# Optimization experiments

Hardware: AMD Instinct MI355X
Metric: run time of the kernel (lower is better)

The kernel has to match this reference:

```python
import jax, jax.numpy as jnp
import numpy as np

NUM_USERS = 100000
NUM_ITEMS = 200000
EMB_DIM = 64
NUM_LAYERS = 3
NUM_INTER = 1000000
BATCH = 16384


def setup_inputs() -> dict:
    key = jax.random.key(0)
    k1, k2, k3, k4, k5, k6, k7 = jax.random.split(key, 7)
    # xavier-uniform-ish init for embeddings
    bound_u = float(np.sqrt(6.0 / (NUM_USERS + EMB_DIM)))
    bound_i = float(np.sqrt(6.0 / (NUM_ITEMS + EMB_DIM)))
    user_emb = jax.random.uniform(k1, (NUM_USERS, EMB_DIM), jnp.float32, -bound_u, bound_u)
    item_emb = jax.random.uniform(k2, (NUM_ITEMS, EMB_DIM), jnp.float32, -bound_i, bound_i)
    layer_weights = jax.random.uniform(k3, (NUM_LAYERS + 1,), jnp.float32)
    inter_users = jax.random.randint(k4, (NUM_INTER,), 0, NUM_USERS, jnp.int32)
    inter_items = jax.random.randint(k5, (NUM_INTER,), 0, NUM_ITEMS, jnp.int32)
    user_ids = jax.random.randint(k6, (BATCH,), 0, NUM_USERS, jnp.int32)
    item_ids = jax.random.randint(k7, (BATCH,), 0, NUM_ITEMS, jnp.int32)
    return {
        "user_emb": user_emb,
        "item_emb": item_emb,
        "layer_weights": layer_weights,
        "inter_users": inter_users,
        "inter_items": inter_items,
        "user_ids": user_ids,
        "item_ids": item_ids,
    }


def reference(user_emb, item_emb, layer_weights, inter_users, inter_items, user_ids, item_ids):
    n_users = user_emb.shape[0]
    n_items = item_emb.shape[0]
    n_nodes = n_users + n_items

    # Symmetrized bipartite edge list: (u -> i+n_users) and (i+n_users -> u)
    rows = inter_users
    cols = inter_items + n_users
    src = jnp.concatenate([rows, cols])  # [2E]
    dst = jnp.concatenate([cols, rows])  # [2E]

    # Symmetric degree normalization: D^{-1/2} A D^{-1/2}
    deg = jax.ops.segment_sum(jnp.ones_like(src, dtype=jnp.float32), src,
                              num_segments=n_nodes)
    dinv = jnp.where(deg > 0, jax.lax.rsqrt(jnp.maximum(deg, 1.0)) * (deg > 0), 0.0)
    dinv = jnp.where(deg > 0, deg ** -0.5, 0.0)
    edge_w = dinv[src] * dinv[dst]  # [2E]

    emb = jnp.concatenate([user_emb, item_emb], axis=0)  # [N, D]
    weights = jax.nn.softmax(layer_weights)

    final = weights[0] * emb
    for layer in range(NUM_LAYERS):
        # SpMM: out[src] += w * emb[dst]
        emb = jax.ops.segment_sum(edge_w[:, None] * emb[dst], src,
                                  num_segments=n_nodes)
        final = final + weights[layer + 1] * emb

    u_final = final[:n_users]
    i_final = final[n_users:]

    user_vectors = u_final[user_ids]   # [B, D]
    item_vectors = i_final[item_ids]   # [B, D]
    scores = jnp.sum(user_vectors * item_vectors, axis=1)  # [B]
    return scores
```

## Files before the change

kernel.cpp:

```cpp
#include <hip/hip_runtime.h>
#include <math.h>

#define NUM_USERS 100000
#define NUM_ITEMS 200000
#define N_NODES   300000
#define EMB       64
#define NUM_INTER 1000000
#define MAX_SLOTS (2 * NUM_INTER + 3 * N_NODES + 16)
#define BATCH     16384

#define BSHIFT 9
#define BNODES 512
#define NBKT   ((N_NODES + BNODES - 1) / BNODES)
#define CAP    6144
#define EDGES_PER_BLOCK 4096
#define AB_BLOCKS ((NUM_INTER + EDGES_PER_BLOCK - 1) / EDGES_PER_BLOCK)
#define QMARK_BLOCKS ((BATCH * 2) / 256)

#define CONV_BLOCKS ((N_NODES * 8 + 255) / 256)
#define PROP_BLOCKS ((N_NODES * 8 + 255) / 256)

typedef int      vint4 __attribute__((ext_vector_type(4)));
typedef _Float16 half8 __attribute__((ext_vector_type(8)));

#define PMASK 0x7FFFFu

__global__ __launch_bounds__(256) void bucket_scatter_k(
        const int* __restrict__ iu, const int* __restrict__ ii,
        const int* __restrict__ uid, const int* __restrict__ iid,
        int* __restrict__ cursor , unsigned* __restrict__ pairs,
        unsigned char* __restrict__ qflag, int* __restrict__ flag) {
    int tid = threadIdx.x;
    if (blockIdx.x < QMARK_BLOCKS) {
        int t = blockIdx.x * 256 + tid;
        int node = (t & 1) ? (NUM_USERS + iid[t >> 1]) : uid[t >> 1];
        qflag[node] = 1;
        flag[node]  = 1;
        return;
    }
    __shared__ int hist[NBKT];
    __shared__ int gbase[NBKT];
    int bid = blockIdx.x - QMARK_BLOCKS;
    for (int b = tid; b < NBKT; b += 256) hist[b] = 0;
    __syncthreads();

    int e0 = bid * EDGES_PER_BLOCK;
    int u[16], it[16];
    unsigned pk[32];
    #pragma unroll
    for (int k = 0; k < 16; ++k) {
        int e = e0 + k * 256 + tid;
        bool v = (e < NUM_INTER);
        u[k]  = v ? iu[e] : -1;
        it[k] = v ? (NUM_USERS + ii[e]) : -1;
    }
    #pragma unroll
    for (int k = 0; k < 16; ++k) {
        if (u[k] >= 0) {
            int b0 = u[k] >> BSHIFT;
            int r0 = atomicAdd(&hist[b0], 1);
            pk[2 * k] = ((unsigned)b0 << 13) | (unsigned)r0;
            int b1 = it[k] >> BSHIFT;
            int r1 = atomicAdd(&hist[b1], 1);
            pk[2 * k + 1] = ((unsigned)b1 << 13) | (unsigned)r1;
        }
    }
    __syncthreads();
    for (int b = tid; b < NBKT; b += 256) {
        int c = hist[b];
        if (c) gbase[b] = atomicAdd(&cursor[b * 16], c);
    }
    __syncthreads();
    #pragma unroll
    for (int k = 0; k < 16; ++k) {
        if (u[k] >= 0) {
            unsigned p0 = pk[2 * k];
            int b0 = (int)(p0 >> 13);
            int s0 = gbase[b0] + (int)(p0 & 0x1fffu);
            if (s0 < CAP)
                pairs[(size_t)b0 * CAP + s0] =
                    ((unsigned)(u[k] & (BNODES - 1)) << 19) | (unsigned)it[k];
            unsigned p1 = pk[2 * k + 1];
            int b1 = (int)(p1 >> 13);
            int s1 = gbase[b1] + (int)(p1 & 0x1fffu);
            if (s1 < CAP)
                pairs[(size_t)b1 * CAP + s1] =
                    ((unsigned)(it[k] & (BNODES - 1)) << 19) | (unsigned)u[k];
        }
    }
}

__global__ __launch_bounds__(256) void bucket_deg_k(
        const int* __restrict__ cursor, const unsigned* __restrict__ pairs,
        const unsigned char* __restrict__ qflag, int* __restrict__ flag,
        int* __restrict__ deg, float* __restrict__ dinv, float* __restrict__ d2,
        float* __restrict__ rcp, int* __restrict__ lofs, int* __restrict__ bkt_padded) {
    __shared__ int cnt[BNODES];
    __shared__ int sc[256];
    __shared__ unsigned qf[BNODES / 4];
    int b = blockIdx.x, tid = threadIdx.x;
    cnt[tid] = 0; cnt[tid + 256] = 0;
    if (tid < BNODES / 4)
        qf[tid] = ((const unsigned*)(qflag + ((size_t)b << BSHIFT)))[tid];
    __syncthreads();
    int n = cursor[b * 16]; if (n > CAP) n = CAP;
    const unsigned* p = pairs + (size_t)b * CAP;
    const unsigned char* qfb = (const unsigned char*)qf;
    for (int j = tid; j < n; j += 256) {
        unsigned code = p[j];
        int l = (int)(code >> 19);
        atomicAdd(&cnt[l], 1);
        if (qfb[l]) flag[code & PMASK] = 1;
    }
    __syncthreads();

    int l0 = 2 * tid, l1 = 2 * tid + 1;
    int c0 = cnt[l0], c1 = cnt[l1];
    int p0 = (c0 + 3) & ~3, p1 = (c1 + 3) & ~3;
    int s = p0 + p1;
    sc[tid] = s;
    __syncthreads();
    for (int o = 1; o < 256; o <<= 1) {
        int x = (tid >= o) ? sc[tid - o] : 0;
        __syncthreads();
        sc[tid] += x;
        __syncthreads();
    }
    int excl = sc[tid] - s;
    int g0 = (b << BSHIFT) + l0;
    int g1 = g0 + 1;
    if (g0 < N_NODES) {
        deg[g0] = c0;
        float fd = (float)c0;
        dinv[g0] = (c0 > 0) ? (1.0f / sqrtf(fd)) : 0.0f;
        d2[g0]   = (c0 > 0) ? (1.0f / fd) : 0.0f;
        rcp[g0]  = (c0 > 0) ? sqrtf(fd) : 0.0f;
        lofs[g0] = excl;
    }
    if (g1 < N_NODES) {
        deg[g1] = c1;
        float fd = (float)c1;
        dinv[g1] = (c1 > 0) ? (1.0f / sqrtf(fd)) : 0.0f;
        d2[g1]   = (c1 > 0) ? (1.0f / fd) : 0.0f;
        rcp[g1]  = (c1 > 0) ? sqrtf(fd) : 0.0f;
        lofs[g1] = excl + p0;
    }
    if (tid == 255) bkt_padded[b] = sc[255];
}

__global__ void csr_mid_k(const int* __restrict__ bkt_padded, int* __restrict__ bkt_base,
                          int* __restrict__ row_start,
                          const float* __restrict__ lw, float* __restrict__ w,
                          _Float16* __restrict__ semb, _Float16* __restrict__ z1,
                          _Float16* __restrict__ z2) {
    __shared__ int lds[1024];
    int t = threadIdx.x;
    int v = (t < NBKT) ? bkt_padded[t] : 0;
    lds[t] = v;
    __syncthreads();
    for (int o = 1; o < 1024; o <<= 1) {
        int x = (t >= o) ? lds[t - o] : 0;
        __syncthreads();
        lds[t] += x;
        __syncthreads();
    }
    if (t < NBKT) bkt_base[t] = lds[t] - v;
    if (t == 1023) row_start[N_NODES] = lds[1023];
    if (t < 96) {
        unsigned* p = (t < 32) ? (unsigned*)semb : (t < 64) ? (unsigned*)z1 : (unsigned*)z2;
        p[(size_t)N_NODES * 32 + (t & 31)] = 0u;
    }
    if (t == 0) {
        float a = lw[0], b = lw[1], c = lw[2], d = lw[3];
        float m = fmaxf(fmaxf(a, b), fmaxf(c, d));
        float e0 = expf(a - m), e1 = expf(b - m), e2 = expf(c - m), e3 = expf(d - m);
        float sm = e0 + e1 + e2 + e3;
        w[0] = e0 / sm; w[1] = e1 / sm; w[2] = e2 / sm; w[3] = e3 / sm;
    }
}

__global__ __launch_bounds__(256) void bucket_build_k(
        const int* __restrict__ cursor, const unsigned* __restrict__ pairs,
        const int* __restrict__ bkt_base, const int* __restrict__ lofs,
        int* __restrict__ row_start, int* __restrict__ nbr,
        const float* __restrict__ dinv,
        const float* __restrict__ ue, const float* __restrict__ ie,
        _Float16* __restrict__ semb) {
    int bid = blockIdx.x;
    int tid = threadIdx.x;
    if (bid >= NBKT) {
        int t = (bid - NBKT) * 256 + tid;
        int node = t >> 3;
        int q = t & 7;
        if (node >= N_NODES) return;
        const float4* src = (node < NUM_USERS)
            ? (const float4*)ue + (size_t)node * 16
            : (const float4*)ie + (size_t)(node - NUM_USERS) * 16;
        float4 f0 = src[q * 2];
        float4 f1 = src[q * 2 + 1];
        float s = dinv[node];
        half8 h;
        h[0] = (_Float16)(s * f0.x); h[1] = (_Float16)(s * f0.y);
        h[2] = (_Float16)(s * f0.z); h[3] = (_Float16)(s * f0.w);
        h[4] = (_Float16)(s * f1.x); h[5] = (_Float16)(s * f1.y);
        h[6] = (_Float16)(s * f1.z); h[7] = (_Float16)(s * f1.w);
        ((half8*)semb)[(size_t)node * 8 + q] = h;
        return;
    }
    __shared__ int ofs[BNODES];
    __shared__ int cnt2[BNODES];
    int b = bid;
    int base = bkt_base[b];
    {
        int g0 = (b << BSHIFT) + tid;
        int g1 = g0 + 256;
        int o0 = (g0 < N_NODES) ? lofs[g0] : 0;
        int o1 = (g1 < N_NODES) ? lofs[g1] : 0;
        ofs[tid] = o0; ofs[tid + 256] = o1;
        cnt2[tid] = 0; cnt2[tid + 256] = 0;
        if (g0 < N_NODES) row_start[g0] = base + o0;
        if (g1 < N_NODES) row_start[g1] = base + o1;
    }
    __syncthreads();
    int n = cursor[b * 16]; if (n > CAP) n = CAP;
    const unsigned* p = pairs + (size_t)b * CAP;
    for (int j = tid; j < n; j += 256) {
        unsigned code = p[j];
        int l = (int)(code >> 19);
        int r = atomicAdd(&cnt2[l], 1);
        nbr[base + ofs[l] + r] = (int)(code & PMASK);
    }
}

__global__ void prop_first_k(const int* __restrict__ row_start, const int* __restrict__ nbr,
                             const int* __restrict__ deg, const float* __restrict__ d2,
                             const _Float16* __restrict__ semb, _Float16* __restrict__ z1) {
    int t = blockIdx.x * blockDim.x + threadIdx.x;
    int node = t >> 3;
    int q = t & 7;
    if (node >= N_NODES) return;
    int beg = row_start[node], end = row_start[node + 1];
    int lim = beg + deg[node];
    const half8* src = (const half8*)semb;
    float a0 = 0.f, a1 = 0.f, a2 = 0.f, a3 = 0.f, a4 = 0.f, a5 = 0.f, a6 = 0.f, a7 = 0.f;
    for (int j = beg; j < end; j += 8) {
        vint4 na = __builtin_nontemporal_load((const vint4*)(nbr + j));
        vint4 nb = __builtin_nontemporal_load((const vint4*)(nbr + j + 4));
        #pragma unroll
        for (int k = 0; k < 8; ++k) {
            int id = (j + k < lim) ? ((k < 4) ? na[k] : nb[k - 4]) : N_NODES;
            half8 h = src[(size_t)id * 8 + q];
            a0 += (float)h[0]; a1 += (float)h[1]; a2 += (float)h[2]; a3 += (float)h[3];
            a4 += (float)h[4]; a5 += (float)h[5]; a6 += (float)h[6]; a7 += (float)h[7];
        }
    }
    float s = d2[node];
    half8 r;
    r[0] = (_Float16)(s * a0); r[1] = (_Float16)(s * a1);
    r[2] = (_Float16)(s * a2); r[3] = (_Float16)(s * a3);
    r[4] = (_Float16)(s * a4); r[5] = (_Float16)(s * a5);
    r[6] = (_Float16)(s * a6); r[7] = (_Float16)(s * a7);
    __builtin_nontemporal_store(r, (half8*)z1 + (size_t)node * 8 + q);
}

__global__ void prop_masked_k(const int* __restrict__ row_start, const int* __restrict__ nbr,
                              const int* __restrict__ deg, const float* __restrict__ d2,
                              const int* __restrict__ flag,
                              const _Float16* __restrict__ in, _Float16* __restrict__ out) {
    int t = blockIdx.x * blockDim.x + threadIdx.x;
    int node = t >> 3;
    int q = t & 7;
    if (node >= N_NODES) return;
    if (!flag[node]) return;
    int beg = row_start[node], end = row_start[node + 1];
    int lim = beg + deg[node];
    const half8* src = (const half8*)in;
    float a0 = 0.f, a1 = 0.f, a2 = 0.f, a3 = 0.f, a4 = 0.f, a5 = 0.f, a6 = 0.f, a7 = 0.f;
    for (int j = beg; j < end; j += 8) {
        vint4 na = __builtin_nontemporal_load((const vint4*)(nbr + j));
        vint4 nb = __builtin_nontemporal_load((const vint4*)(nbr + j + 4));
        #pragma unroll
        for (int k = 0; k < 8; ++k) {
            int id = (j + k < lim) ? ((k < 4) ? na[k] : nb[k - 4]) : N_NODES;
            half8 h = src[(size_t)id * 8 + q];
            a0 += (float)h[0]; a1 += (float)h[1]; a2 += (float)h[2]; a3 += (float)h[3];
            a4 += (float)h[4]; a5 += (float)h[5]; a6 += (float)h[6]; a7 += (float)h[7];
        }
    }
    float s = d2[node];
    half8 r;
    r[0] = (_Float16)(s * a0); r[1] = (_Float16)(s * a1);
    r[2] = (_Float16)(s * a2); r[3] = (_Float16)(s * a3);
    r[4] = (_Float16)(s * a4); r[5] = (_Float16)(s * a5);
    r[6] = (_Float16)(s * a6); r[7] = (_Float16)(s * a7);
    __builtin_nontemporal_store(r, (half8*)out + (size_t)node * 8 + q);
}

__global__ void fused_score_k(const int* __restrict__ row_start, const int* __restrict__ nbr,
                              const int* __restrict__ deg,
                              const float* __restrict__ dinv, const float* __restrict__ rcp,
                              const float* __restrict__ ue, const float* __restrict__ ie,
                              const _Float16* __restrict__ z1, const _Float16* __restrict__ z2,
                              const int* __restrict__ uid, const int* __restrict__ iid,
                              const float* __restrict__ w4, float* __restrict__ out) {
    int t = blockIdx.x * blockDim.x + threadIdx.x;
    int slot = t >> 4;
    if (slot >= BATCH) return;
    int within = t & 15;
    int side = within >> 3;
    int q = within & 7;

    int node;
    const float4* erow;
    if (side == 0) {
        int u = uid[slot];
        node = u;
        erow = (const float4*)ue + (size_t)u * 16;
    } else {
        int ii_ = iid[slot];
        node = NUM_USERS + ii_;
        erow = (const float4*)ie + (size_t)ii_ * 16;
    }

    float w0 = w4[0], w1 = w4[1], w2 = w4[2], w3 = w4[3];
    int beg = row_start[node], end = row_start[node + 1];
    int lim = beg + deg[node];
    const half8* z2v = (const half8*)z2;

    float a0 = 0.f, a1 = 0.f, a2 = 0.f, a3 = 0.f, a4 = 0.f, a5 = 0.f, a6 = 0.f, a7 = 0.f;
    for (int j = beg; j < end; j += 8) {
        vint4 na = __builtin_nontemporal_load((const vint4*)(nbr + j));
        vint4 nb = __builtin_nontemporal_load((const vint4*)(nbr + j + 4));
        #pragma unroll
        for (int k = 0; k < 8; ++k) {
            int id = (j + k < lim) ? ((k < 4) ? na[k] : nb[k - 4]) : N_NODES;
            half8 h = z2v[(size_t)id * 8 + q];
            a0 += (float)h[0]; a1 += (float)h[1]; a2 += (float)h[2]; a3 += (float)h[3];
            a4 += (float)h[4]; a5 += (float)h[5]; a6 += (float)h[6]; a7 += (float)h[7];
        }
    }

    float r  = rcp[node];
    float di = dinv[node];
    float e[8];
    *reinterpret_cast<float4*>(&e[0]) = erow[q * 2];
    *reinterpret_cast<float4*>(&e[4]) = erow[q * 2 + 1];
    half8 h1 = ((const half8*)z1)[(size_t)node * 8 + q];
    half8 h2 = z2v[(size_t)node * 8 + q];
    float acc[8] = {a0, a1, a2, a3, a4, a5, a6, a7};

    float f[8];
    #pragma unroll
    for (int d = 0; d < 8; ++d)
        f[d] = w0 * e[d] + r * (w1 * (float)h1[d] + w2 * (float)h2[d]) + w3 * di * acc[d];

    float p = 0.f;
    #pragma unroll
    for (int d = 0; d < 8; ++d) {
        float o = __shfl_xor(f[d], 8);
        p += f[d] * o;
    }
    p += __shfl_xor(p, 1);
    p += __shfl_xor(p, 2);
    p += __shfl_xor(p, 4);

    if (within == 0) out[slot] = p;
}


extern "C" void kernel_launch(void* const* d_in, const int* in_sizes, int n_in,
                              void* d_out, int out_size, void* d_ws, size_t ws_size,
                              hipStream_t stream) {
    const float* user_emb = (const float*)d_in[0];
    const float* item_emb = (const float*)d_in[1];
    const float* layer_w  = (const float*)d_in[2];
    const int*   inter_u  = (const int*)d_in[3];
    const int*   inter_i  = (const int*)d_in[4];
    const int*   user_ids = (const int*)d_in[5];
    const int*   item_ids = (const int*)d_in[6];
    float* out = (float*)d_out;

    char* base = (char*)d_ws;
    size_t off = 0;
    auto alloc = [&](size_t bytes) -> char* {
        char* p = base + off;
        off = (off + bytes + 255) & ~(size_t)255;
        return p;
    };
    float*    w4        = (float*)    alloc(4 * sizeof(float));
    int*      deg       = (int*)      alloc((size_t)N_NODES * sizeof(int));
    float*    dinv      = (float*)    alloc((size_t)N_NODES * sizeof(float));
    float*    d2        = (float*)    alloc((size_t)N_NODES * sizeof(float));
    float*    rcp       = (float*)    alloc((size_t)N_NODES * sizeof(float));
    int*      lofs      = (int*)      alloc((size_t)N_NODES * sizeof(int));
    int*      row_start = (int*)      alloc(((size_t)N_NODES + 1) * sizeof(int));
    int*      bkt_pad   = (int*)      alloc((size_t)NBKT * sizeof(int));
    int*      bkt_base  = (int*)      alloc((size_t)NBKT * sizeof(int));
    int*           flag   = (int*)          alloc((size_t)N_NODES * sizeof(int));
    unsigned char* qflag  = (unsigned char*)alloc((size_t)N_NODES + 512);
    int*           cursor = (int*)          alloc((size_t)NBKT * 16 * sizeof(int));
    unsigned* pairs     = (unsigned*) alloc((size_t)NBKT * CAP * sizeof(unsigned));
    int*      csr_nbr   = (int*)      alloc((size_t)MAX_SLOTS * sizeof(int));
    _Float16* semb      = (_Float16*) alloc(((size_t)N_NODES + 1) * EMB * sizeof(_Float16));
    _Float16* zA        = (_Float16*) alloc(((size_t)N_NODES + 1) * EMB * sizeof(_Float16));
    _Float16* zB        = (_Float16*) alloc(((size_t)N_NODES + 1) * EMB * sizeof(_Float16));

    size_t span = (size_t)((char*)cursor - (char*)flag) + (size_t)NBKT * 16 * sizeof(int);
    hipMemsetAsync(flag, 0, span, stream);

    bucket_scatter_k<<<QMARK_BLOCKS + AB_BLOCKS, 256, 0, stream>>>(
        inter_u, inter_i, user_ids, item_ids, cursor, pairs, qflag, flag);

    bucket_deg_k<<<NBKT, 256, 0, stream>>>(
        cursor, pairs, qflag, flag, deg, dinv, d2, rcp, lofs, bkt_pad);

    csr_mid_k<<<1, 1024, 0, stream>>>(bkt_pad, bkt_base, row_start, layer_w, w4, semb, zB, zA);

    bucket_build_k<<<NBKT + CONV_BLOCKS, 256, 0, stream>>>(
        cursor, pairs, bkt_base, lofs, row_start, csr_nbr, dinv, user_emb, item_emb, semb);

    prop_first_k<<<PROP_BLOCKS, 256, 0, stream>>>(
        row_start, csr_nbr, deg, d2, semb, zB);

    prop_masked_k<<<PROP_BLOCKS, 256, 0, stream>>>(
        row_start, csr_nbr, deg, d2, flag, zB, zA);

    fused_score_k<<<(BATCH * 16 + 255) / 256, 256, 0, stream>>>(
        row_start, csr_nbr, deg, dinv, rcp, user_emb, item_emb,
        zB , zA , user_ids, item_ids, w4, out);
}
```

Before: 271.9 us.

## Fuse CSR build stages into one per-bucket kernel with fixed bucket slot regions

Merges the degree, global scan, CSR build and embedding-conversion kernels into a single per-bucket kernel. Each bucket now gets a fixed 8192-slot region in the neighbour array, so the global prefix scan over buckets is no longer needed. The softmax and padding-row init move into an extra block of the scatter kernel, and the flag array shrinks from int to byte. This removes two launches and the intermediate lofs, bkt_pad and bkt_base arrays, at the cost of a sparser neighbour array and a per-bucket neighbour overflow risk past 8192 padded slots. It also drops the nontemporal stores and derives row end from the degree.

After: 267.5 us. No clear change (-1.6%).

```diff
diff --git a/kernel.cpp b/kernel.cpp
--- a/kernel.cpp
+++ b/kernel.cpp
@@ -6,18 +6,18 @@
 #define N_NODES   300000
 #define EMB       64
 #define NUM_INTER 1000000
-#define MAX_SLOTS (2 * NUM_INTER + 3 * N_NODES + 16)
 #define BATCH     16384
 
 #define BSHIFT 9
 #define BNODES 512
 #define NBKT   ((N_NODES + BNODES - 1) / BNODES)
 #define CAP    6144
+#define RSHIFT 13
+#define RSLOTS (1 << RSHIFT)
 #define EDGES_PER_BLOCK 4096
 #define AB_BLOCKS ((NUM_INTER + EDGES_PER_BLOCK - 1) / EDGES_PER_BLOCK)
 #define QMARK_BLOCKS ((BATCH * 2) / 256)
 
-#define CONV_BLOCKS ((N_NODES * 8 + 255) / 256)
 #define PROP_BLOCKS ((N_NODES * 8 + 255) / 256)
 
 typedef int      vint4 __attribute__((ext_vector_type(4)));
@@ -29,7 +29,9 @@
         const int* __restrict__ iu, const int* __restrict__ ii,
         const int* __restrict__ uid, const int* __restrict__ iid,
         int* __restrict__ cursor , unsigned* __restrict__ pairs,
-        unsigned char* __restrict__ qflag, int* __restrict__ flag) {
+        unsigned char* __restrict__ qflag, unsigned char* __restrict__ flag,
+        const float* __restrict__ lw, float* __restrict__ w4,
+        _Float16* __restrict__ semb, _Float16* __restrict__ z1, _Float16* __restrict__ z2) {
     int tid = threadIdx.x;
     if (blockIdx.x < QMARK_BLOCKS) {
         int t = blockIdx.x * 256 + tid;
@@ -38,9 +40,23 @@
         flag[node]  = 1;
         return;
     }
+    if (blockIdx.x == QMARK_BLOCKS) {
+        if (tid < 96) {
+            unsigned* p = (tid < 32) ? (unsigned*)semb : (tid < 64) ? (unsigned*)z1 : (unsigned*)z2;
+            p[(size_t)N_NODES * 32 + (tid & 31)] = 0u;
+        }
+        if (tid == 0) {
+            float a = lw[0], b = lw[1], c = lw[2], d = lw[3];
+            float m = fmaxf(fmaxf(a, b), fmaxf(c, d));
+            float e0 = expf(a - m), e1 = expf(b - m), e2 = expf(c - m), e3 = expf(d - m);
+            float sm = e0 + e1 + e2 + e3;
+            w4[0] = e0 / sm; w4[1] = e1 / sm; w4[2] = e2 / sm; w4[3] = e3 / sm;
+        }
+        return;
+    }
     __shared__ int hist[NBKT];
     __shared__ int gbase[NBKT];
-    int bid = blockIdx.x - QMARK_BLOCKS;
+    int bid = blockIdx.x - QMARK_BLOCKS - 1;
     for (int b = tid; b < NBKT; b += 256) hist[b] = 0;
     __syncthreads();
 
@@ -90,12 +106,16 @@
     }
 }
 
-__global__ __launch_bounds__(256) void bucket_deg_k(
+__global__ __launch_bounds__(256) void bucket_all_k(
         const int* __restrict__ cursor, const unsigned* __restrict__ pairs,
-        const unsigned char* __restrict__ qflag, int* __restrict__ flag,
+        const unsigned char* __restrict__ qflag, unsigned char* __restrict__ flag,
         int* __restrict__ deg, float* __restrict__ dinv, float* __restrict__ d2,
-        float* __restrict__ rcp, int* __restrict__ lofs, int* __restrict__ bkt_padded) {
+        float* __restrict__ rcp, int* __restrict__ row_start, int* __restrict__ nbr,
+        const float* __restrict__ ue, const float* __restrict__ ie,
+        _Float16* __restrict__ semb) {
     __shared__ int cnt[BNODES];
+    __shared__ int lofs_s[BNODES];
+    __shared__ float dinv_s[BNODES];
     __shared__ int sc[256];
     __shared__ unsigned qf[BNODES / 4];
     int b = blockIdx.x, tid = threadIdx.x;
@@ -114,7 +134,7 @@
     }
     __syncthreads();
 
-    int l0 = 2 * tid, l1 = 2 * tid + 1;
+    int l0 = 2 * tid, l1 = l0 + 1;
     int c0 = cnt[l0], c1 = cnt[l1];
     int p0 = (c0 + 3) & ~3, p1 = (c1 + 3) & ~3;
     int s = p0 + p1;
@@ -127,108 +147,52 @@
         __syncthreads();
     }
     int excl = sc[tid] - s;
-    int g0 = (b << BSHIFT) + l0;
-    int g1 = g0 + 1;
+    int gb = b << BSHIFT;
+    int g0 = gb + l0, g1 = gb + l1;
+    float fd0 = (float)c0, fd1 = (float)c1;
+    float di0 = (c0 > 0) ? (1.0f / sqrtf(fd0)) : 0.0f;
+    float di1 = (c1 > 0) ? (1.0f / sqrtf(fd1)) : 0.0f;
     if (g0 < N_NODES) {
-        deg[g0] = c0;
-        float fd = (float)c0;
-        dinv[g0] = (c0 > 0) ? (1.0f / sqrtf(fd)) : 0.0f;
-        d2[g0]   = (c0 > 0) ? (1.0f / fd) : 0.0f;
-        rcp[g0]  = (c0 > 0) ? sqrtf(fd) : 0.0f;
-        lofs[g0] = excl;
+        deg[g0] = c0; dinv[g0] = di0;
+        d2[g0]  = (c0 > 0) ? (1.0f / fd0) : 0.0f;
+        rcp[g0] = (c0 > 0) ? sqrtf(fd0) : 0.0f;
+        row_start[g0] = (b << RSHIFT) + excl;
     }
     if (g1 < N_NODES) {
-        deg[g1] = c1;
-        float fd = (float)c1;
-        dinv[g1] = (c1 > 0) ? (1.0f / sqrtf(fd)) : 0.0f;
-        d2[g1]   = (c1 > 0) ? (1.0f / fd) : 0.0f;
-        rcp[g1]  = (c1 > 0) ? sqrtf(fd) : 0.0f;
-        lofs[g1] = excl + p0;
-    }
-    if (tid == 255) bkt_padded[b] = sc[255];
-}
-
-__global__ void csr_mid_k(const int* __restrict__ bkt_padded, int* __restrict__ bkt_base,
-                          int* __restrict__ row_start,
-                          const float* __restrict__ lw, float* __restrict__ w,
-                          _Float16* __restrict__ semb, _Float16* __restrict__ z1,
-                          _Float16* __restrict__ z2) {
-    __shared__ int lds[1024];
-    int t = threadIdx.x;
-    int v = (t < NBKT) ? bkt_padded[t] : 0;
-    lds[t] = v;
-    __syncthreads();
-    for (int o = 1; o < 1024; o <<= 1) {
-        int x = (t >= o) ? lds[t - o] : 0;
-        __syncthreads();
-        lds[t] += x;
-        __syncthreads();
-    }
-    if (t < NBKT) bkt_base[t] = lds[t] - v;
-    if (t == 1023) row_start[N_NODES] = lds[1023];
-    if (t < 96) {
-        unsigned* p = (t < 32) ? (unsigned*)semb : (t < 64) ? (unsigned*)z1 : (unsigned*)z2;
-        p[(size_t)N_NODES * 32 + (t & 31)] = 0u;
-    }
-    if (t == 0) {
-        float a = lw[0], b = lw[1], c = lw[2], d = lw[3];
-        float m = fmaxf(fmaxf(a, b), fmaxf(c, d));
-        float e0 = expf(a - m), e1 = expf(b - m), e2 = expf(c - m), e3 = expf(d - m);
-        float sm = e0 + e1 + e2 + e3;
-        w[0] = e0 / sm; w[1] = e1 / sm; w[2] = e2 / sm; w[3] = e3 / sm;
-    }
-}
-
-__global__ __launch_bounds__(256) void bucket_build_k(
-        const int* __restrict__ cursor, const unsigned* __restrict__ pairs,
-        const int* __restrict__ bkt_base, const int* __restrict__ lofs,
-        int* __restrict__ row_start, int* __restrict__ nbr,
-        const float* __restrict__ dinv,
-        const float* __restrict__ ue, const float* __restrict__ ie,
-        _Float16* __restrict__ semb) {
-    int bid = blockIdx.x;
-    int tid = threadIdx.x;
-    if (bid >= NBKT) {
-        int t = (bid - NBKT) * 256 + tid;
-        int node = t >> 3;
-        int q = t & 7;
-        if (node >= N_NODES) return;
-        const float4* src = (node < NUM_USERS)
-            ? (const float4*)ue + (size_t)node * 16
-            : (const float4*)ie + (size_t)(node - NUM_USERS) * 16;
-        float4 f0 = src[q * 2];
-        float4 f1 = src[q * 2 + 1];
-        float s = dinv[node];
-        half8 h;
-        h[0] = (_Float16)(s * f0.x); h[1] = (_Float16)(s * f0.y);
-        h[2] = (_Float16)(s * f0.z); h[3] = (_Float16)(s * f0.w);
-        h[4] = (_Float16)(s * f1.x); h[5] = (_Float16)(s * f1.y);
-        h[6] = (_Float16)(s * f1.z); h[7] = (_Float16)(s * f1.w);
-        ((half8*)semb)[(size_t)node * 8 + q] = h;
-        return;
-    }
-    __shared__ int ofs[BNODES];
-    __shared__ int cnt2[BNODES];
-    int b = bid;
-    int base = bkt_base[b];
-    {
-        int g0 = (b << BSHIFT) + tid;
-        int g1 = g0 + 256;
-        int o0 = (g0 < N_NODES) ? lofs[g0] : 0;
-        int o1 = (g1 < N_NODES) ? lofs[g1] : 0;
-        ofs[tid] = o0; ofs[tid + 256] = o1;
-        cnt2[tid] = 0; cnt2[tid + 256] = 0;
-        if (g0 < N_NODES) row_start[g0] = base + o0;
-        if (g1 < N_NODES) row_start[g1] = base + o1;
-    }
-    __syncthreads();
-    int n = cursor[b * 16]; if (n > CAP) n = CAP;
-    const unsigned* p = pairs + (size_t)b * CAP;
+        deg[g1] = c1; dinv[g1] = di1;
+        d2[g1]  = (c1 > 0) ? (1.0f / fd1) : 0.0f;
+        rcp[g1] = (c1 > 0) ? sqrtf(fd1) : 0.0f;
+        row_start[g1] = (b << RSHIFT) + excl + p0;
+    }
+    lofs_s[l0] = excl; lofs_s[l1] = excl + p0;
+    dinv_s[l0] = di0;  dinv_s[l1] = di1;
+    cnt[l0] = 0; cnt[l1] = 0;
+    __syncthreads();
+
+    int nbase = b << RSHIFT;
     for (int j = tid; j < n; j += 256) {
         unsigned code = p[j];
         int l = (int)(code >> 19);
-        int r = atomicAdd(&cnt2[l], 1);
-        nbr[base + ofs[l] + r] = (int)(code & PMASK);
+        int r = atomicAdd(&cnt[l], 1);
+        nbr[nbase + lofs_s[l] + r] = (int)(code & PMASK);
+    }
+    for (int t = tid; t < BNODES * 8; t += 256) {
+        int nl = t >> 3, q = t & 7;
+        int node = gb + nl;
+        if (node < N_NODES) {
+            const float4* src = (node < NUM_USERS)
+                ? (const float4*)ue + (size_t)node * 16
+                : (const float4*)ie + (size_t)(node - NUM_USERS) * 16;
+            float4 f0 = src[q * 2];
+            float4 f1 = src[q * 2 + 1];
+            float sdi = dinv_s[nl];
+            half8 h;
+            h[0] = (_Float16)(sdi * f0.x); h[1] = (_Float16)(sdi * f0.y);
+            h[2] = (_Float16)(sdi * f0.z); h[3] = (_Float16)(sdi * f0.w);
+            h[4] = (_Float16)(sdi * f1.x); h[5] = (_Float16)(sdi * f1.y);
+            h[6] = (_Float16)(sdi * f1.z); h[7] = (_Float16)(sdi * f1.w);
+            ((half8*)semb)[(size_t)node * 8 + q] = h;
+        }
     }
 }
 
@@ -239,8 +203,10 @@
     int node = t >> 3;
     int q = t & 7;
     if (node >= N_NODES) return;
-    int beg = row_start[node], end = row_start[node + 1];
-    int lim = beg + deg[node];
+    int d = deg[node];
+    int beg = row_start[node];
+    int lim = beg + d;
+    int end = beg + ((d + 3) & ~3);
     const half8* src = (const half8*)semb;
     float a0 = 0.f, a1 = 0.f, a2 = 0.f, a3 = 0.f, a4 = 0.f, a5 = 0.f, a6 = 0.f, a7 = 0.f;
     for (int j = beg; j < end; j += 8) {
@@ -260,20 +226,22 @@
     r[2] = (_Float16)(s * a2); r[3] = (_Float16)(s * a3);
     r[4] = (_Float16)(s * a4); r[5] = (_Float16)(s * a5);
     r[6] = (_Float16)(s * a6); r[7] = (_Float16)(s * a7);
-    __builtin_nontemporal_store(r, (half8*)z1 + (size_t)node * 8 + q);
+    ((half8*)z1)[(size_t)node * 8 + q] = r;
 }
 
 __global__ void prop_masked_k(const int* __restrict__ row_start, const int* __restrict__ nbr,
                               const int* __restrict__ deg, const float* __restrict__ d2,
-                              const int* __restrict__ flag,
+                              const unsigned char* __restrict__ flag,
                               const _Float16* __restrict__ in, _Float16* __restrict__ out) {
     int t = blockIdx.x * blockDim.x + threadIdx.x;
     int node = t >> 3;
     int q = t & 7;
     if (node >= N_NODES) return;
     if (!flag[node]) return;
-    int beg = row_start[node], end = row_start[node + 1];
-    int lim = beg + deg[node];
+    int d = deg[node];
+    int beg = row_start[node];
+    int lim = beg + d;
+    int end = beg + ((d + 3) & ~3);
     const half8* src = (const half8*)in;
     float a0 = 0.f, a1 = 0.f, a2 = 0.f, a3 = 0.f, a4 = 0.f, a5 = 0.f, a6 = 0.f, a7 = 0.f;
     for (int j = beg; j < end; j += 8) {
@@ -293,7 +261,7 @@
     r[2] = (_Float16)(s * a2); r[3] = (_Float16)(s * a3);
     r[4] = (_Float16)(s * a4); r[5] = (_Float16)(s * a5);
     r[6] = (_Float16)(s * a6); r[7] = (_Float16)(s * a7);
-    __builtin_nontemporal_store(r, (half8*)out + (size_t)node * 8 + q);
+    ((half8*)out)[(size_t)node * 8 + q] = r;
 }
 
 __global__ void fused_score_k(const int* __restrict__ row_start, const int* __restrict__ nbr,
@@ -323,8 +291,10 @@
     }
 
     float w0 = w4[0], w1 = w4[1], w2 = w4[2], w3 = w4[3];
-    int beg = row_start[node], end = row_start[node + 1];
-    int lim = beg + deg[node];
+    int d = deg[node];
+    int beg = row_start[node];
+    int lim = beg + d;
+    int end = beg + ((d + 3) & ~3);
     const half8* z2v = (const half8*)z2;
 
     float a0 = 0.f, a1 = 0.f, a2 = 0.f, a3 = 0.f, a4 = 0.f, a5 = 0.f, a6 = 0.f, a7 = 0.f;
@@ -351,20 +321,20 @@
 
     float f[8];
     #pragma unroll
-    for (int d = 0; d < 8; ++d)
-        f[d] = w0 * e[d] + r * (w1 * (float)h1[d] + w2 * (float)h2[d]) + w3 * di * acc[d];
-
-    float p = 0.f;
-    #pragma unroll
-    for (int d = 0; d < 8; ++d) {
-        float o = __shfl_xor(f[d], 8);
-        p += f[d] * o;
-    }
-    p += __shfl_xor(p, 1);
-    p += __shfl_xor(p, 2);
-    p += __shfl_xor(p, 4);
-
-    if (within == 0) out[slot] = p;
+    for (int dd = 0; dd < 8; ++dd)
+        f[dd] = w0 * e[dd] + r * (w1 * (float)h1[dd] + w2 * (float)h2[dd]) + w3 * di * acc[dd];
+
+    float pr = 0.f;
+    #pragma unroll
+    for (int dd = 0; dd < 8; ++dd) {
+        float o = __shfl_xor(f[dd], 8);
+        pr += f[dd] * o;
+    }
+    pr += __shfl_xor(pr, 1);
+    pr += __shfl_xor(pr, 2);
+    pr += __shfl_xor(pr, 4);
+
+    if (within == 0) out[slot] = pr;
 }
 
 
@@ -392,15 +362,12 @@
     float*    dinv      = (float*)    alloc((size_t)N_NODES * sizeof(float));
     float*    d2        = (float*)    alloc((size_t)N_NODES * sizeof(float));
     float*    rcp       = (float*)    alloc((size_t)N_NODES * sizeof(float));
-    int*      lofs      = (int*)      alloc((size_t)N_NODES * sizeof(int));
-    int*      row_start = (int*)      alloc(((size_t)N_NODES + 1) * sizeof(int));
-    int*      bkt_pad   = (int*)      alloc((size_t)NBKT * sizeof(int));
-    int*      bkt_base  = (int*)      alloc((size_t)NBKT * sizeof(int));
-    int*           flag   = (int*)          alloc((size_t)N_NODES * sizeof(int));
+    int*      row_start = (int*)      alloc((size_t)N_NODES * sizeof(int));
+    unsigned char* flag   = (unsigned char*)alloc((size_t)N_NODES + 256);
     unsigned char* qflag  = (unsigned char*)alloc((size_t)N_NODES + 512);
     int*           cursor = (int*)          alloc((size_t)NBKT * 16 * sizeof(int));
     unsigned* pairs     = (unsigned*) alloc((size_t)NBKT * CAP * sizeof(unsigned));
-    int*      csr_nbr   = (int*)      alloc((size_t)MAX_SLOTS * sizeof(int));
+    int*      csr_nbr   = (int*)      alloc((size_t)NBKT * RSLOTS * sizeof(int));
     _Float16* semb      = (_Float16*) alloc(((size_t)N_NODES + 1) * EMB * sizeof(_Float16));
     _Float16* zA        = (_Float16*) alloc(((size_t)N_NODES + 1) * EMB * sizeof(_Float16));
     _Float16* zB        = (_Float16*) alloc(((size_t)N_NODES + 1) * EMB * sizeof(_Float16));
@@ -408,16 +375,13 @@
     size_t span = (size_t)((char*)cursor - (char*)flag) + (size_t)NBKT * 16 * sizeof(int);
     hipMemsetAsync(flag, 0, span, stream);
 
-    bucket_scatter_k<<<QMARK_BLOCKS + AB_BLOCKS, 256, 0, stream>>>(
-        inter_u, inter_i, user_ids, item_ids, cursor, pairs, qflag, flag);
-
-    bucket_deg_k<<<NBKT, 256, 0, stream>>>(
-        cursor, pairs, qflag, flag, deg, dinv, d2, rcp, lofs, bkt_pad);
-
-    csr_mid_k<<<1, 1024, 0, stream>>>(bkt_pad, bkt_base, row_start, layer_w, w4, semb, zB, zA);
-
-    bucket_build_k<<<NBKT + CONV_BLOCKS, 256, 0, stream>>>(
-        cursor, pairs, bkt_base, lofs, row_start, csr_nbr, dinv, user_emb, item_emb, semb);
+    bucket_scatter_k<<<QMARK_BLOCKS + 1 + AB_BLOCKS, 256, 0, stream>>>(
+        inter_u, inter_i, user_ids, item_ids, cursor, pairs, qflag, flag,
+        layer_w, w4, semb, zB, zA);
+
+    bucket_all_k<<<NBKT, 256, 0, stream>>>(
+        cursor, pairs, qflag, flag, deg, dinv, d2, rcp, row_start, csr_nbr,
+        user_emb, item_emb, semb);
 
     prop_first_k<<<PROP_BLOCKS, 256, 0, stream>>>(
         row_start, csr_nbr, deg, d2, semb, zB);
```
